# Kernel tuning notes

Measured on AMD Instinct MI355X. Metric: run time of the kernel, lower is better.

Reference implementation:

```python
import jax, jax.numpy as jnp
import numpy as np

B, T, C, H, M, R = 2, 2048, 768, 6, 3072, 320
D = C // H  # head_dim = 128


def setup_inputs() -> dict:
    key = jax.random.key(0)
    ks = jax.random.split(key, 11)
    s = 0.02
    return {
        "x": jax.random.normal(ks[0], (B, T, C), jnp.float32),
        "forward_memory": jax.random.normal(ks[1], (B, M, C), jnp.float32),
        "reverse_memory": jax.random.normal(ks[2], (B, R, C), jnp.float32),
        "ctrl": jax.random.uniform(ks[3], (5,), jnp.float32),
        "Wq": jax.random.normal(ks[4], (C, C), jnp.float32) * s,
        "Wk": jax.random.normal(ks[5], (C, C), jnp.float32) * s,
        "Wv": jax.random.normal(ks[6], (C, C), jnp.float32) * s,
        "Wo": jax.random.normal(ks[7], (C, C), jnp.float32) * s,
        "Wc": jax.random.normal(ks[8], (C, 5), jnp.float32) * 1e-4,  # ctrl_init_scale
        "Wg": jax.random.normal(ks[9], (H, C), jnp.float32) * s,
        "bg": jnp.full((H,), -1.0, jnp.float32),  # gate_bias_init
    }


def reference(x, forward_memory, reverse_memory, ctrl, Wq, Wk, Wv, Wo, Wc, Wg, bg):
    Bx, Tx, Cx = x.shape
    Hx = bg.shape[0]
    Dx = Cx // Hx
    # query with control-vector fusion (ctrl broadcast to every token)
    q = x @ Wq.T + ctrl @ Wc.T  # [B,T,C]
    # concat local tokens with forward+reverse memory, project K/V once
    kv_in = jnp.concatenate([x, forward_memory, reverse_memory], axis=1)  # [B,S,C]
    k = kv_in @ Wk.T
    v = kv_in @ Wv.T

    def heads(t):
        return t.reshape(Bx, -1, Hx, Dx).transpose(0, 2, 1, 3)  # [B,H,*,D]

    qh, kh, vh = heads(q), heads(k), heads(v)
    S = kh.shape[2]
    scores = jnp.einsum("bhtd,bhsd->bhts", qh, kh) * (Dx ** -0.5)
    # causal mask over local block only; memory columns always visible
    causal = jnp.triu(jnp.ones((Tx, Tx), bool), 1)
    mask = jnp.concatenate([causal, jnp.zeros((Tx, S - Tx), bool)], axis=1)
    scores = jnp.where(mask, jnp.float32(-1e30), scores)
    w = jax.nn.softmax(scores, axis=-1)  # [B,H,T,S]
    # split attention output into local and memory contributions
    local = jnp.einsum("bhts,bhsd->bhtd", w[..., :Tx], vh[:, :, :Tx])
    mem = jnp.einsum("bhts,bhsd->bhtd", w[..., Tx:], vh[:, :, Tx:])
    # per-head sigmoid gate on the memory path, computed from the fused query
    gate = jax.nn.sigmoid(q @ Wg.T + bg)  # [B,T,H]
    gate = gate.transpose(0, 2, 1)[..., None]  # [B,H,T,1]
    out = local + gate * mem
    out = out.transpose(0, 2, 1, 3).reshape(Bx, Tx, Cx)
    return out @ Wo.T
```

## Files before the change

### kernel.cpp

```cpp
#include <hip/hip_runtime.h>


typedef unsigned short u16;
typedef unsigned int   u32;
typedef __bf16 bf16x8 __attribute__((ext_vector_type(8)));
typedef float  f32x4  __attribute__((ext_vector_type(4)));

#define B_ 2
#define T_ 2048
#define C_ 768
#define H_ 6
#define D_ 128
#define M_ 3072
#define R_ 320
#define S_ 5440
#define BT_ 4096
#define BS_ 10880
#define NS_ 3
#define NMEM_ 53

#define GLDS(src, dst) __builtin_amdgcn_global_load_lds( \
    (const __attribute__((address_space(1))) void*)(src), \
    (__attribute__((address_space(3))) void*)(dst), 16, 0, 0)

__device__ __forceinline__ float b2f(u16 u) {
  union { u32 i; float f; } c; c.i = ((u32)u) << 16; return c.f;
}
__device__ __forceinline__ u16 f2b(float f) {
  union { float f; u32 i; } c; c.f = f;
  return (u16)((c.i + 0x7FFFu + ((c.i >> 16) & 1u)) >> 16);
}

__global__ __launch_bounds__(256) void k_cast4(const float* __restrict__ s0,
                                               const float* __restrict__ s1,
                                               const float* __restrict__ s2,
                                               const float* __restrict__ s3,
                                               u16* __restrict__ d0,
                                               u16* __restrict__ d1,
                                               u16* __restrict__ d2,
                                               u16* __restrict__ d3) {
  const float* src = (blockIdx.y == 0) ? s0 : (blockIdx.y == 1) ? s1
                   : (blockIdx.y == 2) ? s2 : s3;
  u16* dst = (blockIdx.y == 0) ? d0 : (blockIdx.y == 1) ? d1
           : (blockIdx.y == 2) ? d2 : d3;
  int i = (blockIdx.x * 256 + threadIdx.x) * 4;
  float4 v = *(const float4*)(src + i);
  u16 o[4] = { f2b(v.x), f2b(v.y), f2b(v.z), f2b(v.w) };
  *(ushort4*)(dst + i) = *(ushort4*)o;
}

__global__ __launch_bounds__(256) void k_concat(const float* __restrict__ x,
                                                const float* __restrict__ fm,
                                                const float* __restrict__ rm,
                                                u16* __restrict__ kv) {
  long long i = ((long long)blockIdx.x * 256 + threadIdx.x) * 8;
  if (i >= (long long)BS_ * C_) return;
  int row = (int)(i / C_);
  int col = (int)(i - (long long)row * C_);
  int b = row / S_, s = row - b * S_;
  const float* src;
  if (s < T_)           src = x  + (size_t)(b * T_ + s) * C_ + col;
  else if (s < T_ + M_) src = fm + (size_t)(b * M_ + (s - T_)) * C_ + col;
  else                  src = rm + (size_t)(b * R_ + (s - T_ - M_)) * C_ + col;
  float4 a0 = *(const float4*)src;
  float4 a1 = *(const float4*)(src + 4);
  u16 o[8] = { f2b(a0.x), f2b(a0.y), f2b(a0.z), f2b(a0.w),
               f2b(a1.x), f2b(a1.y), f2b(a1.z), f2b(a1.w) };
  *(uint4*)(kv + i) = *(uint4*)o;
}

template<bool F32OUT, bool QCBIAS>
__global__ __launch_bounds__(256) void k_gemm(const u16* __restrict__ A,
                                              const u16* __restrict__ W,
                                              const float* __restrict__ ctrl,
                                              const float* __restrict__ Wc,
                                              void* __restrict__ outv,
                                              int rows, int rowShift, int bstride) {
  __shared__ __align__(16) u16 As[3][128 * 32];
  __shared__ __align__(16) u16 Bs[3][128 * 32];
  const int t = threadIdx.x;
  const int lane = t & 63, wv = t >> 6;
  const int wr = (wv >> 1) * 64, wc = (wv & 1) * 64;
  const int fr = lane & 15, fq = lane >> 4;
  const int rowTile = blockIdx.x * 128;
  const int colTile = blockIdx.y * 128;

  f32x4 acc[4][4] = {};

  const int e0 = t * 8;
  const int e1 = (256 + t) * 8;
  const int r0 = e0 >> 5, c0 = e0 & 31;
  const int r1 = e1 >> 5, c1 = e1 & 31;

  int gr0 = rowTile + r0; if (gr0 >= rows) gr0 = rows - 1;
  int gr1 = rowTile + r1; if (gr1 >= rows) gr1 = rows - 1;
  const int msk = (1 << rowShift) - 1;
  const size_t pr0 = (size_t)(gr0 >> rowShift) * bstride + (gr0 & msk);
  const size_t pr1 = (size_t)(gr1 >> rowShift) * bstride + (gr1 & msk);
  const u16* gaB0 = A + pr0 * C_ + c0;
  const u16* gaB1 = A + pr1 * C_ + c1;
  const u16* gbB0 = W + (size_t)(colTile + r0) * C_ + c0;
  const u16* gbB1 = W + (size_t)(colTile + r1) * C_ + c1;
  const int aOff0 = (wv * 64) * 8, aOff1 = (256 + wv * 64) * 8;

#define STAGE_G(bi, kt) do { \
    GLDS(gaB0 + (kt), &As[bi][aOff0]); \
    GLDS(gaB1 + (kt), &As[bi][aOff1]); \
    GLDS(gbB0 + (kt), &Bs[bi][aOff0]); \
    GLDS(gbB1 + (kt), &Bs[bi][aOff1]); } while (0)

  STAGE_G(0, 0);
  STAGE_G(1, 32);
  int cur = 0;

  for (int kt = 0; kt < C_; kt += 32) {
    int nx2 = cur + 2; if (nx2 >= 3) nx2 -= 3;
    if (kt + 64 < C_) {
      STAGE_G(nx2, kt + 64);
      asm volatile("s_waitcnt vmcnt(8)" ::: "memory");
    } else if (kt + 32 < C_) {
      asm volatile("s_waitcnt vmcnt(4)" ::: "memory");
    } else {
      asm volatile("s_waitcnt vmcnt(0)" ::: "memory");
    }
    __builtin_amdgcn_s_barrier();

    bf16x8 af[4], bfr[4];
#pragma unroll
    for (int i = 0; i < 4; ++i) af[i]  = *(const bf16x8*)&As[cur][(wr + i * 16 + fr) * 32 + fq * 8];
#pragma unroll
    for (int i = 0; i < 4; ++i) bfr[i] = *(const bf16x8*)&Bs[cur][(wc + i * 16 + fr) * 32 + fq * 8];
#pragma unroll
    for (int mi = 0; mi < 4; ++mi)
#pragma unroll
      for (int ni = 0; ni < 4; ++ni)
        acc[mi][ni] = __builtin_amdgcn_mfma_f32_16x16x32_bf16(af[mi], bfr[ni], acc[mi][ni], 0, 0, 0);
    __builtin_amdgcn_s_barrier();
    cur = (cur == 2) ? 0 : cur + 1;
  }
#undef STAGE_G

#pragma unroll
  for (int mi = 0; mi < 4; ++mi) {
#pragma unroll
    for (int ni = 0; ni < 4; ++ni) {
      int cc = colTile + wc + ni * 16 + fr;
      float bb = 0.f;
      if (QCBIAS) {
#pragma unroll
        for (int j = 0; j < 5; ++j) bb += ctrl[j] * Wc[cc * 5 + j];
      }
#pragma unroll
      for (int j = 0; j < 4; ++j) {
        int rr = rowTile + wr + mi * 16 + fq * 4 + j;
        if (rr < rows) {
          float val = acc[mi][ni][j] + bb;
          if (F32OUT) ((float*)outv)[(size_t)rr * C_ + cc] = val;
          else        ((u16*)outv)[(size_t)rr * C_ + cc] = f2b(val);
        }
      }
    }
  }
}

__global__ __launch_bounds__(256) void k_gemmT(const u16* __restrict__ kvb,
                                               const u16* __restrict__ W,
                                               u16* __restrict__ vt) {
  __shared__ __align__(16) u16 Ws[3][128 * 32];
  __shared__ __align__(16) u16 Xs[3][128 * 32];
  const int t = threadIdx.x;
  const int lane = t & 63, wv = t >> 6;
  const int wr = (wv >> 1) * 64, wc = (wv & 1) * 64;
  const int fr = lane & 15, fq = lane >> 4;
  const int sTile = blockIdx.x * 128;
  const int ccTile = blockIdx.y * 128;
  const int b = blockIdx.z;

  f32x4 acc[4][4] = {};

  const int e0 = t * 8;
  const int e1 = (256 + t) * 8;
  const int r0 = e0 >> 5, c0 = e0 & 31;
  const int r1 = e1 >> 5, c1 = e1 & 31;

  int gs0 = sTile + r0; if (gs0 >= S_) gs0 = S_ - 1;
  int gs1 = sTile + r1; if (gs1 >= S_) gs1 = S_ - 1;
  const u16* gxB0 = kvb + (size_t)(b * S_ + gs0) * C_ + c0;
  const u16* gxB1 = kvb + (size_t)(b * S_ + gs1) * C_ + c1;
  const u16* gwB0 = W + (size_t)(ccTile + r0) * C_ + c0;
  const u16* gwB1 = W + (size_t)(ccTile + r1) * C_ + c1;
  const int aOff0 = (wv * 64) * 8, aOff1 = (256 + wv * 64) * 8;

#define STAGE_T(bi, kt) do { \
    GLDS(gwB0 + (kt), &Ws[bi][aOff0]); \
    GLDS(gwB1 + (kt), &Ws[bi][aOff1]); \
    GLDS(gxB0 + (kt), &Xs[bi][aOff0]); \
    GLDS(gxB1 + (kt), &Xs[bi][aOff1]); } while (0)

  STAGE_T(0, 0);
  STAGE_T(1, 32);
  int cur = 0;

  for (int kt = 0; kt < C_; kt += 32) {
    int nx2 = cur + 2; if (nx2 >= 3) nx2 -= 3;
    if (kt + 64 < C_) {
      STAGE_T(nx2, kt + 64);
      asm volatile("s_waitcnt vmcnt(8)" ::: "memory");
    } else if (kt + 32 < C_) {
      asm volatile("s_waitcnt vmcnt(4)" ::: "memory");
    } else {
      asm volatile("s_waitcnt vmcnt(0)" ::: "memory");
    }
    __builtin_amdgcn_s_barrier();

    bf16x8 wf[4], xf[4];
#pragma unroll
    for (int i = 0; i < 4; ++i) wf[i] = *(const bf16x8*)&Ws[cur][(wr + i * 16 + fr) * 32 + fq * 8];
#pragma unroll
    for (int i = 0; i < 4; ++i) xf[i] = *(const bf16x8*)&Xs[cur][(wc + i * 16 + fr) * 32 + fq * 8];
#pragma unroll
    for (int mi = 0; mi < 4; ++mi)
#pragma unroll
      for (int ni = 0; ni < 4; ++ni)
        acc[mi][ni] = __builtin_amdgcn_mfma_f32_16x16x32_bf16(wf[mi], xf[ni], acc[mi][ni], 0, 0, 0);
    __builtin_amdgcn_s_barrier();
    cur = (cur == 2) ? 0 : cur + 1;
  }
#undef STAGE_T

#pragma unroll
  for (int mi = 0; mi < 4; ++mi) {
#pragma unroll
    for (int ni = 0; ni < 4; ++ni) {
      int ss = sTile + wc + ni * 16 + fr;
      if (ss < S_) {
#pragma unroll
        for (int j = 0; j < 4; ++j) {
          int cc = ccTile + wr + mi * 16 + fq * 4 + j;
          vt[((size_t)(b * C_ + cc)) * S_ + ss] = f2b(acc[mi][ni][j]);
        }
      }
    }
  }
}

__global__ __launch_bounds__(256) void k_gate(const u16* __restrict__ q,
                                              const float* __restrict__ Wg,
                                              const float* __restrict__ bg,
                                              float* __restrict__ gate) {
  int gid = blockIdx.x * 4 + (threadIdx.x >> 6);
  int lane = threadIdx.x & 63;
  int h = gid % H_;
  int bt = gid / H_;
  const u16* qrow = q + (size_t)bt * C_;
  const float* wrow = Wg + (size_t)h * C_;
  float a = 0.f;
#pragma unroll
  for (int i = 0; i < 12; ++i) {
    int e = i * 64 + lane;
    a += b2f(qrow[e]) * wrow[e];
  }
#pragma unroll
  for (int off = 1; off < 64; off <<= 1) a += __shfl_xor(a, off);
  if (lane == 0) {
    float xg = a + bg[h];
    int b = bt / T_, tt = bt - b * T_;
    gate[((size_t)b * H_ + h) * T_ + tt] = 1.f / (1.f + __expf(-xg));
  }
}

__global__ __launch_bounds__(512, 4) void k_attn6(const u16* __restrict__ q,
                                                  const u16* __restrict__ kk,
                                                  const u16* __restrict__ vt,
                                                  const float* __restrict__ gate,
                                                  u16* __restrict__ pacc0,
                                                  u16* __restrict__ pacc1,
                                                  u16* __restrict__ pacc2,
                                                  float* __restrict__ pl) {
  __shared__ __align__(16) u16 Ks[2][64 * 128];
  __shared__ __align__(16) u16 Vs[128 * 64];
  __shared__ __align__(16) u16 Pb[8][16 * 64];

  const int bh = blockIdx.x;
  const int b = bh / H_, h = bh - b * H_;
  const int y = blockIdx.y, c = blockIdx.z;
  const int wv = threadIdx.x >> 6, lane = threadIdx.x & 63;
  const int fr = lane & 15, fq = lane >> 4;
  const int qbase = y * 128 + wv * 16;
  u16* P = Pb[wv];

  const u16* Qh = q + (size_t)(b * T_ + qbase) * C_ + h * D_;
  const float* gh = gate + ((size_t)b * H_ + h) * T_ + qbase;

  const int kRow0 = wv * 8 + (lane >> 4), kRow1 = kRow0 + 4;
  const int kCol0 = (((lane & 15) * 16) ^ ((kRow0 & 7) << 4)) >> 1;
  const int kCol1 = (((lane & 15) * 16) ^ ((kRow1 & 7) << 4)) >> 1;
  const u16* kSrc0 = kk + (size_t)(b * S_ + kRow0) * C_ + h * D_ + kCol0;
  const u16* kSrc1 = kk + (size_t)(b * S_ + kRow1) * C_ + h * D_ + kCol1;
  const int vRow0 = wv * 16 + (lane >> 3), vRow1 = vRow0 + 8;
  const int vCol0 = (((lane & 7) * 16) ^ ((vRow0 & 7) << 4)) >> 1;
  const int vCol1 = (((lane & 7) * 16) ^ ((vRow1 & 7) << 4)) >> 1;
  const u16* vSrc0 = vt + ((size_t)b * C_ + h * D_ + vRow0) * S_ + vCol0;
  const u16* vSrc1 = vt + ((size_t)b * C_ + h * D_ + vRow1) * S_ + vCol1;

  bf16x8 qf[4];
#pragma unroll
  for (int kc = 0; kc < 4; ++kc)
    qf[kc] = *(const bf16x8*)&Qh[(size_t)fr * C_ + kc * 32 + fq * 8];

  f32x4 acc[8] = {};
  f32x4 accL = {}, accM = {};
  float g4[4], lg[4];
#pragma unroll
  for (int r = 0; r < 4; ++r) { g4[r] = gh[fq * 4 + r]; lg[r] = __log2f(g4[r]); }

  const __bf16 one_h = (__bf16)1.0f;
  bf16x8 ones = { one_h, one_h, one_h, one_h, one_h, one_h, one_h, one_h };

  const float scl = 0.08838834764831845f * 1.4426950408889634f;
  const int xk = (fr & 7) << 4;

  const int nloc = 2 * y + 2;
  const int ntot = nloc + NMEM_;
  auto s_of = [&](int i) { return (i < nloc) ? i * 64 : T_ + (i - nloc) * 64; };

  {
    int s0 = s_of(c);
    GLDS(kSrc0 + (size_t)s0 * C_, &Ks[0][(wv * 8) * 128]);
    GLDS(kSrc1 + (size_t)s0 * C_, &Ks[0][(wv * 8 + 4) * 128]);
  }
  int cur = 0;

  for (int i = c; i < ntot; i += NS_) {
    const int s0 = s_of(i);
    const bool haveNext = (i + NS_ < ntot);
    GLDS(vSrc0 + s0, &Vs[(wv * 16) * 64]);
    GLDS(vSrc1 + s0, &Vs[(wv * 16 + 8) * 64]);
    if (haveNext) {
      int sn = s_of(i + NS_);
      GLDS(kSrc0 + (size_t)sn * C_, &Ks[cur ^ 1][(wv * 8) * 128]);
      GLDS(kSrc1 + (size_t)sn * C_, &Ks[cur ^ 1][(wv * 8 + 4) * 128]);
      asm volatile("s_waitcnt vmcnt(4)" ::: "memory");
    } else {
      asm volatile("s_waitcnt vmcnt(2)" ::: "memory");
    }
    __builtin_amdgcn_s_barrier();

    const bool loc = (i < nloc);
    const bool maskedStep = loc && (s0 + 63 > qbase);
    const bool skip = loc && (s0 > qbase + 15);

    bf16x8 pa0, pa1;
    if (!skip) {
      f32x4 sc[4] = {{}, {}, {}, {}};
#pragma unroll
      for (int quad = 0; quad < 4; ++quad) {
        const u16* Krow = &Ks[cur][(quad * 16 + fr) * 128];
#pragma unroll
        for (int kc = 0; kc < 4; ++kc) {
          bf16x8 kf = *(const bf16x8*)&Krow[((kc * 64 + fq * 16) ^ xk) >> 1];
          sc[quad] = __builtin_amdgcn_mfma_f32_16x16x32_bf16(qf[kc], kf, sc[quad], 0, 0, 0);
        }
      }
      if (maskedStep) {
#pragma unroll
        for (int quad = 0; quad < 4; ++quad)
#pragma unroll
          for (int r = 0; r < 4; ++r)
            if (s0 + quad * 16 + fr > qbase + fq * 4 + r) sc[quad][r] = -1.0e30f;
      }
      float ca[4];
#pragma unroll
      for (int r = 0; r < 4; ++r) ca[r] = loc ? 0.f : lg[r];
#pragma unroll
      for (int quad = 0; quad < 4; ++quad)
#pragma unroll
        for (int r = 0; r < 4; ++r) {
          float p = exp2f(fmaf(sc[quad][r], scl, ca[r]));
          ((__bf16*)P)[(fq * 4 + r) * 64 + quad * 16 + fr] = (__bf16)p;
        }
      __builtin_amdgcn_wave_barrier();
      pa0 = *(const bf16x8*)&P[fr * 64 + fq * 8];
      pa1 = *(const bf16x8*)&P[fr * 64 + 32 + fq * 8];
    }
    if (haveNext) asm volatile("s_waitcnt vmcnt(2)" ::: "memory");
    else          asm volatile("s_waitcnt vmcnt(0)" ::: "memory");
    __builtin_amdgcn_s_barrier();
    if (!skip) {
#pragma unroll
      for (int nt = 0; nt < 8; ++nt) {
        const u16* Vrow = &Vs[(nt * 16 + fr) * 64];
        bf16x8 vf0 = *(const bf16x8*)&Vrow[((fq * 16) ^ xk) >> 1];
        bf16x8 vf1 = *(const bf16x8*)&Vrow[((64 + fq * 16) ^ xk) >> 1];
        acc[nt] = __builtin_amdgcn_mfma_f32_16x16x32_bf16(pa0, vf0, acc[nt], 0, 0, 0);
        acc[nt] = __builtin_amdgcn_mfma_f32_16x16x32_bf16(pa1, vf1, acc[nt], 0, 0, 0);
      }
      if (loc) {
        accL = __builtin_amdgcn_mfma_f32_16x16x32_bf16(pa0, ones, accL, 0, 0, 0);
        accL = __builtin_amdgcn_mfma_f32_16x16x32_bf16(pa1, ones, accL, 0, 0, 0);
      } else {
        accM = __builtin_amdgcn_mfma_f32_16x16x32_bf16(pa0, ones, accM, 0, 0, 0);
        accM = __builtin_amdgcn_mfma_f32_16x16x32_bf16(pa1, ones, accM, 0, 0, 0);
      }
    }
    __builtin_amdgcn_s_barrier();
    cur ^= 1;
  }

  u16* pb = (c == 0) ? pacc0 : (c == 1) ? pacc1 : pacc2;
  const size_t rowb = (size_t)bh * T_ + qbase;
#pragma unroll
  for (int nt = 0; nt < 8; ++nt)
#pragma unroll
    for (int r = 0; r < 4; ++r)
      pb[(rowb + fq * 4 + r) * D_ + nt * 16 + fr] = f2b(acc[nt][r]);
  if (fr == 0) {
#pragma unroll
    for (int r = 0; r < 4; ++r)
      pl[((size_t)c * (B_ * H_) + bh) * T_ + qbase + fq * 4 + r] =
          accL[r] + accM[r] / g4[r];
  }
}

__global__ __launch_bounds__(256) void k_combine(const u16* __restrict__ pacc0,
                                                 const u16* __restrict__ pacc1,
                                                 const u16* __restrict__ pacc2,
                                                 const float* __restrict__ pl,
                                                 u16* __restrict__ ao) {
  const int row = blockIdx.x * 4 + (threadIdx.x >> 6);
  const int lane = threadIdx.x & 63;
  const int bh = row >> 11, t = row & (T_ - 1);
  const int b = bh / H_, h = bh - b * H_;

  float L = pl[(size_t)bh * T_ + t]
          + pl[((size_t)(B_ * H_) + bh) * T_ + t]
          + pl[((size_t)(2 * B_ * H_) + bh) * T_ + t];
  float inv = 1.f / L;
  const size_t rb = ((size_t)bh * T_ + t) * D_ + lane * 2;
  float o0 = 0.f, o1 = 0.f;
  u32 v0 = *(const u32*)&pacc0[rb];
  u32 v1 = *(const u32*)&pacc1[rb];
  u32 v2 = *(const u32*)&pacc2[rb];
  o0 = b2f((u16)(v0 & 0xFFFF)) + b2f((u16)(v1 & 0xFFFF)) + b2f((u16)(v2 & 0xFFFF));
  o1 = b2f((u16)(v0 >> 16)) + b2f((u16)(v1 >> 16)) + b2f((u16)(v2 >> 16));
  u16 o[2] = { f2b(o0 * inv), f2b(o1 * inv) };
  *(u32*)&ao[((size_t)(b * T_ + t)) * C_ + h * D_ + lane * 2] = *(u32*)o;
}

extern "C" void kernel_launch(void* const* d_in, const int* in_sizes, int n_in,
                              void* d_out, int out_size, void* d_ws, size_t ws_size,
                              hipStream_t stream) {
  const float* x   = (const float*)d_in[0];
  const float* fm  = (const float*)d_in[1];
  const float* rm  = (const float*)d_in[2];
  const float* ctl = (const float*)d_in[3];
  const float* Wq  = (const float*)d_in[4];
  const float* Wk  = (const float*)d_in[5];
  const float* Wv  = (const float*)d_in[6];
  const float* Wo  = (const float*)d_in[7];
  const float* Wc  = (const float*)d_in[8];
  const float* Wg  = (const float*)d_in[9];
  const float* bg  = (const float*)d_in[10];
  float* outp = (float*)d_out;

  char* ws = (char*)d_ws;
  float* gate = (float*)(ws + 4096);
  u16* qb    = (u16*)(ws + 102400);
  u16* kv    = (u16*)(ws + 6393856);
  u16* pacc0 = (u16*)(ws + 6393856);
  u16* pacc1 = (u16*)(ws + 12685312);
  u16* kb    = (u16*)(ws + 23105536);
  u16* vt    = (u16*)(ws + 39817216);
  u16* ao    = (u16*)(ws + 39817216);
  u16* pacc2 = (u16*)(ws + 56528896);
  float* pl  = (float*)(ws + 62820352);
  u16* Wqb   = (u16*)(ws + 63115264);
  u16* Wkb   = (u16*)(ws + 64294912);
  u16* Wvb   = (u16*)(ws + 65474560);
  u16* Wob   = (u16*)(ws + 66654208);

  k_cast4<<<dim3(576, 4), dim3(256), 0, stream>>>(Wq, Wk, Wv, Wo,
                                                  Wqb, Wkb, Wvb, Wob);
  k_concat<<<dim3(4080), dim3(256), 0, stream>>>(x, fm, rm, kv);
  k_gemm<false, true><<<dim3(32, 6), dim3(256), 0, stream>>>(
      kv, Wqb, ctl, Wc, qb, BT_, 11, S_);
  k_gemm<false, false><<<dim3(85, 6), dim3(256), 0, stream>>>(
      kv, Wkb, nullptr, nullptr, kb, BS_, 30, 0);
  k_gemmT<<<dim3(43, 6, 2), dim3(256), 0, stream>>>(kv, Wvb, vt);
  k_gate<<<dim3(6144), dim3(256), 0, stream>>>(qb, Wg, bg, gate);
  k_attn6<<<dim3(B_ * H_, 16, NS_), dim3(512), 0, stream>>>(
      qb, kb, vt, gate, pacc0, pacc1, pacc2, pl);
  k_combine<<<dim3(6144), dim3(256), 0, stream>>>(pacc0, pacc1, pacc2, pl, ao);
  k_gemm<true, false><<<dim3(32, 6), dim3(256), 0, stream>>>(
      ao, Wob, nullptr, nullptr, outp, BT_, 30, 0);
}
```

Baseline: 235.1 us.

## Fuse K and V projections into one GEMM kernel sharing activation tiles

Replaces the separate K GEMM and transposed-V GEMM with a single kernel that loads each activation tile once and multiplies it against both Wk and Wv. It writes K row-major and V transposed, using a flattened row index over both batches. This removes one launch and halves activation reads for K/V, at the cost of double accumulator registers, a drop from triple to double buffering, and a 2-block occupancy hint. It also adds s_setprio around the MFMA sections in the attention kernel to favour matrix issue.

```diff
diff --git a/kernel.cpp b/kernel.cpp
--- a/kernel.cpp
+++ b/kernel.cpp
@@ -163,82 +163,98 @@
   }
 }
 
-__global__ __launch_bounds__(256) void k_gemmT(const u16* __restrict__ kvb,
-                                               const u16* __restrict__ W,
-                                               u16* __restrict__ vt) {
-  __shared__ __align__(16) u16 Ws[3][128 * 32];
-  __shared__ __align__(16) u16 Xs[3][128 * 32];
+__global__ __launch_bounds__(256, 2) void k_gemmKV(const u16* __restrict__ kvb,
+                                                   const u16* __restrict__ Wk,
+                                                   const u16* __restrict__ Wv,
+                                                   u16* __restrict__ kb,
+                                                   u16* __restrict__ vt) {
+  __shared__ __align__(16) u16 As[2][128 * 32];
+  __shared__ __align__(16) u16 Ks2[2][128 * 32];
+  __shared__ __align__(16) u16 Vs2[2][128 * 32];
   const int t = threadIdx.x;
   const int lane = t & 63, wv = t >> 6;
   const int wr = (wv >> 1) * 64, wc = (wv & 1) * 64;
   const int fr = lane & 15, fq = lane >> 4;
-  const int sTile = blockIdx.x * 128;
-  const int ccTile = blockIdx.y * 128;
-  const int b = blockIdx.z;
-
-  f32x4 acc[4][4] = {};
+  const int rowTile = blockIdx.x * 128;
+  const int colTile = blockIdx.y * 128;
+
+  f32x4 accK[4][4] = {};
+  f32x4 accV[4][4] = {};
 
   const int e0 = t * 8;
   const int e1 = (256 + t) * 8;
   const int r0 = e0 >> 5, c0 = e0 & 31;
   const int r1 = e1 >> 5, c1 = e1 & 31;
 
-  int gs0 = sTile + r0; if (gs0 >= S_) gs0 = S_ - 1;
-  int gs1 = sTile + r1; if (gs1 >= S_) gs1 = S_ - 1;
-  const u16* gxB0 = kvb + (size_t)(b * S_ + gs0) * C_ + c0;
-  const u16* gxB1 = kvb + (size_t)(b * S_ + gs1) * C_ + c1;
-  const u16* gwB0 = W + (size_t)(ccTile + r0) * C_ + c0;
-  const u16* gwB1 = W + (size_t)(ccTile + r1) * C_ + c1;
+  const u16* gaB0 = kvb + (size_t)(rowTile + r0) * C_ + c0;
+  const u16* gaB1 = kvb + (size_t)(rowTile + r1) * C_ + c1;
+  const u16* gkB0 = Wk + (size_t)(colTile + r0) * C_ + c0;
+  const u16* gkB1 = Wk + (size_t)(colTile + r1) * C_ + c1;
+  const u16* gvB0 = Wv + (size_t)(colTile + r0) * C_ + c0;
+  const u16* gvB1 = Wv + (size_t)(colTile + r1) * C_ + c1;
   const int aOff0 = (wv * 64) * 8, aOff1 = (256 + wv * 64) * 8;
 
-#define STAGE_T(bi, kt) do { \
-    GLDS(gwB0 + (kt), &Ws[bi][aOff0]); \
-    GLDS(gwB1 + (kt), &Ws[bi][aOff1]); \
-    GLDS(gxB0 + (kt), &Xs[bi][aOff0]); \
-    GLDS(gxB1 + (kt), &Xs[bi][aOff1]); } while (0)
-
-  STAGE_T(0, 0);
-  STAGE_T(1, 32);
+#define STAGE_KV(bi, kt) do { \
+    GLDS(gaB0 + (kt), &As[bi][aOff0]); \
+    GLDS(gaB1 + (kt), &As[bi][aOff1]); \
+    GLDS(gkB0 + (kt), &Ks2[bi][aOff0]); \
+    GLDS(gkB1 + (kt), &Ks2[bi][aOff1]); \
+    GLDS(gvB0 + (kt), &Vs2[bi][aOff0]); \
+    GLDS(gvB1 + (kt), &Vs2[bi][aOff1]); } while (0)
+
+  STAGE_KV(0, 0);
   int cur = 0;
 
   for (int kt = 0; kt < C_; kt += 32) {
-    int nx2 = cur + 2; if (nx2 >= 3) nx2 -= 3;
-    if (kt + 64 < C_) {
-      STAGE_T(nx2, kt + 64);
-      asm volatile("s_waitcnt vmcnt(8)" ::: "memory");
-    } else if (kt + 32 < C_) {
-      asm volatile("s_waitcnt vmcnt(4)" ::: "memory");
+    if (kt + 32 < C_) {
+      STAGE_KV(cur ^ 1, kt + 32);
+      asm volatile("s_waitcnt vmcnt(6)" ::: "memory");
     } else {
       asm volatile("s_waitcnt vmcnt(0)" ::: "memory");
     }
     __builtin_amdgcn_s_barrier();
 
-    bf16x8 wf[4], xf[4];
-#pragma unroll
-    for (int i = 0; i < 4; ++i) wf[i] = *(const bf16x8*)&Ws[cur][(wr + i * 16 + fr) * 32 + fq * 8];
-#pragma unroll
-    for (int i = 0; i < 4; ++i) xf[i] = *(const bf16x8*)&Xs[cur][(wc + i * 16 + fr) * 32 + fq * 8];
+    bf16x8 af[4], wkf[4], wvf[4];
+#pragma unroll
+    for (int i = 0; i < 4; ++i) af[i]  = *(const bf16x8*)&As[cur][(wr + i * 16 + fr) * 32 + fq * 8];
+#pragma unroll
+    for (int i = 0; i < 4; ++i) wkf[i] = *(const bf16x8*)&Ks2[cur][(wc + i * 16 + fr) * 32 + fq * 8];
+#pragma unroll
+    for (int i = 0; i < 4; ++i) wvf[i] = *(const bf16x8*)&Vs2[cur][(wc + i * 16 + fr) * 32 + fq * 8];
 #pragma unroll
     for (int mi = 0; mi < 4; ++mi)
 #pragma unroll
-      for (int ni = 0; ni < 4; ++ni)
-        acc[mi][ni] = __builtin_amdgcn_mfma_f32_16x16x32_bf16(wf[mi], xf[ni], acc[mi][ni], 0, 0, 0);
-    __builtin_amdgcn_s_barrier();
-    cur = (cur == 2) ? 0 : cur + 1;
-  }
-#undef STAGE_T
+      for (int ni = 0; ni < 4; ++ni) {
+        accK[mi][ni] = __builtin_amdgcn_mfma_f32_16x16x32_bf16(af[mi], wkf[ni], accK[mi][ni], 0, 0, 0);
+        accV[mi][ni] = __builtin_amdgcn_mfma_f32_16x16x32_bf16(wvf[mi], af[ni], accV[mi][ni], 0, 0, 0);
+      }
+    __builtin_amdgcn_s_barrier();
+    cur ^= 1;
+  }
+#undef STAGE_KV
 
 #pragma unroll
   for (int mi = 0; mi < 4; ++mi) {
 #pragma unroll
     for (int ni = 0; ni < 4; ++ni) {
-      int ss = sTile + wc + ni * 16 + fr;
-      if (ss < S_) {
-#pragma unroll
-        for (int j = 0; j < 4; ++j) {
-          int cc = ccTile + wr + mi * 16 + fq * 4 + j;
-          vt[((size_t)(b * C_ + cc)) * S_ + ss] = f2b(acc[mi][ni][j]);
-        }
+      int cc = colTile + wc + ni * 16 + fr;
+#pragma unroll
+      for (int j = 0; j < 4; ++j) {
+        int rr = rowTile + wr + mi * 16 + fq * 4 + j;
+        kb[(size_t)rr * C_ + cc] = f2b(accK[mi][ni][j]);
+      }
+    }
+  }
+#pragma unroll
+  for (int mi = 0; mi < 4; ++mi) {
+#pragma unroll
+    for (int ni = 0; ni < 4; ++ni) {
+      int sg = rowTile + wr + ni * 16 + fr;
+      int b = sg / S_, s = sg - b * S_;
+#pragma unroll
+      for (int j = 0; j < 4; ++j) {
+        int cc = colTile + wc + mi * 16 + fq * 4 + j;
+        vt[((size_t)(b * C_ + cc)) * S_ + s] = f2b(accV[mi][ni][j]);
       }
     }
   }
@@ -353,6 +369,7 @@
     bf16x8 pa0, pa1;
     if (!skip) {
       f32x4 sc[4] = {{}, {}, {}, {}};
+      __builtin_amdgcn_s_setprio(1);
 #pragma unroll
       for (int quad = 0; quad < 4; ++quad) {
         const u16* Krow = &Ks[cur][(quad * 16 + fr) * 128];
@@ -362,6 +379,7 @@
           sc[quad] = __builtin_amdgcn_mfma_f32_16x16x32_bf16(qf[kc], kf, sc[quad], 0, 0, 0);
         }
       }
+      __builtin_amdgcn_s_setprio(0);
       if (maskedStep) {
 #pragma unroll
         for (int quad = 0; quad < 4; ++quad)
@@ -387,6 +405,7 @@
     else          asm volatile("s_waitcnt vmcnt(0)" ::: "memory");
     __builtin_amdgcn_s_barrier();
     if (!skip) {
+      __builtin_amdgcn_s_setprio(1);
 #pragma unroll
       for (int nt = 0; nt < 8; ++nt) {
         const u16* Vrow = &Vs[(nt * 16 + fr) * 64];
@@ -402,6 +421,7 @@
         accM = __builtin_amdgcn_mfma_f32_16x16x32_bf16(pa0, ones, accM, 0, 0, 0);
         accM = __builtin_amdgcn_mfma_f32_16x16x32_bf16(pa1, ones, accM, 0, 0, 0);
       }
+      __builtin_amdgcn_s_setprio(0);
     }
     __builtin_amdgcn_s_barrier();
     cur ^= 1;
@@ -484,9 +504,7 @@
   k_concat<<<dim3(4080), dim3(256), 0, stream>>>(x, fm, rm, kv);
   k_gemm<false, true><<<dim3(32, 6), dim3(256), 0, stream>>>(
       kv, Wqb, ctl, Wc, qb, BT_, 11, S_);
-  k_gemm<false, false><<<dim3(85, 6), dim3(256), 0, stream>>>(
-      kv, Wkb, nullptr, nullptr, kb, BS_, 30, 0);
-  k_gemmT<<<dim3(43, 6, 2), dim3(256), 0, stream>>>(kv, Wvb, vt);
+  k_gemmKV<<<dim3(85, 6), dim3(256), 0, stream>>>(kv, Wkb, Wvb, kb, vt);
   k_gate<<<dim3(6144), dim3(256), 0, stream>>>(qb, Wg, bg, gate);
   k_attn6<<<dim3(B_ * H_, 16, NS_), dim3(512), 0, stream>>>(
       qb, kb, vt, gate, pacc0, pacc1, pacc2, pl);
```

Result: faster. 217.1 us (-7.7%).
